# Optimization experiments

Hardware: AMD Instinct MI355X
Metric: run time of the kernel (lower is better)

Reference implementation:

```python
import jax, jax.numpy as jnp
import numpy as np

EPS = 1e-4
MP_SILU_C = 0.596
RES_T = 0.3
ATTN_T = 0.3
CLIP = 256.0
HEADS = 8


def normalize(x, dim, eps=EPS):
    # matches torch normalize: x / (eps + sqrt(norm.numel()/x.numel()) * ||x||_dim)
    norm = jnp.sqrt(jnp.sum(jnp.square(x.astype(jnp.float32)), axis=dim, keepdims=True))
    alpha = np.sqrt(norm.size / x.size)
    return x / (eps + alpha * norm).astype(x.dtype)


def mp_silu(x):
    return jax.nn.silu(x) / MP_SILU_C


def mp_sum(a, b, t):
    return (a * (1.0 - t) + b * t) / np.sqrt((1.0 - t) ** 2 + t ** 2)


def mp_conv(x, w, gain=1.0):
    # weight-normalized conv / linear (eval mode: no in-place weight copy)
    w = w.astype(jnp.float32)
    w = normalize(w, tuple(range(1, w.ndim)))
    fan = int(np.prod(w.shape[1:]))
    w = w * (gain / np.sqrt(fan))
    w = w.astype(x.dtype)
    if w.ndim == 2:
        return x @ w.T
    return jax.lax.conv_general_dilated(
        x, w, window_strides=(1, 1), padding='SAME',
        dimension_numbers=('NCHW', 'OIHW', 'NCHW'))


def setup_inputs() -> dict:
    key = jax.random.key(0)
    ks = jax.random.split(key, 8)
    return {
        'x': jax.random.normal(ks[0], (16, 256, 32, 32), jnp.float32),
        'emb': jax.random.normal(ks[1], (16, 1024), jnp.float32),
        'w_skip': jax.random.normal(ks[2], (512, 256, 1, 1), jnp.float32),
        'w_res0': jax.random.normal(ks[3], (512, 512, 3, 3), jnp.float32),
        'w_emb': jax.random.normal(ks[4], (512, 1024), jnp.float32),
        'w_res1': jax.random.normal(ks[5], (512, 512, 3, 3), jnp.float32),
        'w_qkv': jax.random.normal(ks[6], (1536, 512, 1, 1), jnp.float32),
        'w_proj': jax.random.normal(ks[7], (512, 512, 1, 1), jnp.float32),
        'emb_gain': jnp.zeros([], jnp.float32),
    }


def reference(x, emb, w_skip, w_res0, w_emb, w_res1, w_qkv, w_proj, emb_gain):
    # flavor='enc', resample_mode='keep'
    x = mp_conv(x, w_skip)          # conv_skip (in!=out)
    x = normalize(x, 1)             # pixel norm over channels
    y = mp_conv(mp_silu(x), w_res0)
    c = mp_conv(emb, w_emb, gain=emb_gain) + 1.0   # [N, C]
    y = mp_silu(y * c[:, :, None, None].astype(y.dtype))
    y = mp_conv(y, w_res1)
    x = mp_sum(x, y, RES_T)
    # QK-normalized self-attention over H*W tokens
    N, C, H, W = x.shape
    ch = C // HEADS
    y = mp_conv(x, w_qkv)                              # [N, 3C, H, W]
    y = y.reshape(N, HEADS, ch, 3, H * W)
    qkv = normalize(y, 2)                              # L2-normalize per-head channels
    q, k, v = qkv[:, :, :, 0, :], qkv[:, :, :, 1, :], qkv[:, :, :, 2, :]
    attn = jax.nn.softmax(
        jnp.einsum('nhcq,nhck->nhqk', q, k) / np.sqrt(ch), axis=3)
    y = jnp.einsum('nhqk,nhck->nhcq', attn, v).reshape(N, C, H, W)
    y = mp_conv(y, w_proj)
    x = mp_sum(x, y, ATTN_T)
    return jnp.clip(x, -CLIP, CLIP)
```

## Files before the change

kernel.cpp:

```cpp
#include <hip/hip_runtime.h>

typedef unsigned short u16;
typedef unsigned int   u32;
typedef __attribute__((ext_vector_type(8))) short bf16x8;
typedef __attribute__((ext_vector_type(4))) float f32x4;
typedef __attribute__((ext_vector_type(4))) int   int4v;

#define DEV static __device__ __forceinline__

DEV u16 f2b(float f){ u32 u = __builtin_bit_cast(u32,f); u = (u + 0x7FFFu + ((u>>16)&1u))>>16; return (u16)u; }
DEV float b2f(u16 h){ return __builtin_bit_cast(float,(u32)h<<16); }
DEV float mpsilu(float t){ return t/(1.f+__expf(-t)) * 1.6778523489932886f; }
DEV u32 cvtpk(float lo, float hi){ u32 r; asm("v_cvt_pk_bf16_f32 %0, %1, %2" : "=v"(r) : "v"(lo), "v"(hi)); return r; }

DEV void gload16(void* l, const void* g){
  __builtin_amdgcn_global_load_lds(
    (const __attribute__((address_space(1))) void*)g,
    (__attribute__((address_space(3))) void*)l, 16, 0, 0);
}

#define OFF_W0B    0ull
#define OFF_W1B    4718592ull
#define OFF_WSKIPB 9437184ull
#define OFF_WQKVB  9699328ull
#define OFF_WPROJB 11272192ull
#define OFF_WEMB   11796480ull
#define OFF_CEMB   13893632ull
#define OFF_XSKIP  13926400ull
#define OFF_YATT   13926400ull
#define OFF_XNORM  47480832ull
#define OFF_QKVRAW 47480832ull
#define OFF_PAD0   97812480ull
#define OFF_Q      97812480ull
#define OFF_PAD1   116752384ull
#define OFF_V      116752384ull
#define OFF_XB     135692288ull
#define OFF_XRESB  169246720ull
#define OFF_K      186023936ull

__global__ __launch_bounds__(256) void k_prep_weights(
    const float* __restrict__ w_skip, const float* __restrict__ w_res0,
    const float* __restrict__ w_emb,  const float* __restrict__ w_res1,
    const float* __restrict__ w_qkv,  const float* __restrict__ w_proj,
    const float* __restrict__ egain, char* __restrict__ ws)
{
  int b = blockIdx.x, tid = threadIdx.x, lane = tid&63, wid = tid>>6;
  if(b >= 4096){
    int idx = (b-4096)*256 + tid;
    int4v z = {0,0,0,0};
    for(; idx < 270336; idx += 67584){
      int chunk = idx & 63;
      int rest  = idx >> 6;
      int bp    = rest % 132;
      int rest2 = rest / 132;
      int n     = rest2 & 15;
      int buf   = rest2 >> 4;
      int py, px;
      if(bp < 34){ py=0; px=bp; }
      else if(bp < 68){ py=33; px=bp-34; }
      else if(bp < 100){ py=1+(bp-68); px=0; }
      else { py=1+(bp-100); px=33; }
      char* dst = ws + OFF_PAD0 + (size_t)buf*18939904ull
                + ((size_t)n*1156 + (size_t)py*34 + px)*1024 + (chunk<<4);
      *(int4v*)dst = z;
    }
    return;
  }
  const float* src; int fan, mode, o; u16* dstB=nullptr; float* dstF=nullptr; float gain=1.f;
  if(b<512)       { o=b;      src=w_res0+(size_t)o*4608; fan=4608; mode=1; dstB=(u16*)(ws+OFF_W0B); }
  else if(b<1024) { o=b-512;  src=w_res1+(size_t)o*4608; fan=4608; mode=1; dstB=(u16*)(ws+OFF_W1B); }
  else if(b<1536) { o=b-1024; src=w_skip+(size_t)o*256;  fan=256;  mode=0; dstB=(u16*)(ws+OFF_WSKIPB); }
  else if(b<3072) { o=b-1536; src=w_qkv+(size_t)o*512;   fan=512;  mode=0; dstB=(u16*)(ws+OFF_WQKVB); }
  else if(b<3584) { o=b-3072; src=w_proj+(size_t)o*512;  fan=512;  mode=0; dstB=(u16*)(ws+OFF_WPROJB); }
  else            { o=b-3584; src=w_emb+(size_t)o*1024;  fan=1024; mode=2; dstF=(float*)(ws+OFF_WEMB); gain=*egain; }
  float ss=0;
  for(int i=tid;i<fan;i+=256){ float v=src[i]; ss += v*v; }
  for(int i=1;i<64;i<<=1) ss += __shfl_xor(ss,i);
  __shared__ float red[4];
  if(lane==0) red[wid]=ss;
  __syncthreads();
  ss = red[0]+red[1]+red[2]+red[3];
  float scale = gain / (1e-4f*sqrtf((float)fan) + sqrtf(ss));
  if(mode==1){
    for(int t2=tid;t2<4608;t2+=256){
      int tap=t2>>9, c=t2&511;
      dstB[(size_t)tap*262144 + o*512 + c] = f2b(src[c*9+tap]*scale);
    }
  } else {
    for(int i=tid;i<fan;i+=256){
      float v = src[i]*scale;
      if(mode==0) dstB[(size_t)o*fan + i] = f2b(v);
      else dstF[(size_t)o*1024 + i] = v;
    }
  }
}

__global__ __launch_bounds__(256) void k_emb(const float* __restrict__ emb,
    const float* __restrict__ wembs, float* __restrict__ cemb)
{
  int gw = (blockIdx.x*256 + threadIdx.x)>>6, lane = threadIdx.x&63;
  int n = gw>>9, o = gw&511;
  const float* e = emb + (size_t)n*1024;
  const float* w = wembs + (size_t)o*1024;
  float s=0;
  for(int i=lane*4;i<1024;i+=256){
    float4 a=*(const float4*)(e+i), b=*(const float4*)(w+i);
    s += a.x*b.x + a.y*b.y + a.z*b.z + a.w*b.w;
  }
  for(int i=1;i<64;i<<=1) s += __shfl_xor(s,i);
  if(lane==0) cemb[n*512+o] = s + 1.0f;
}

__global__ __launch_bounds__(256) void k_cast_x(const float* __restrict__ x, u16* __restrict__ xb){
  __shared__ u16 t[64*257];
  int bid=blockIdx.x, tid=threadIdx.x;
  int n=bid>>4, p0=(bid&15)<<6;
  int p=tid&63, c0=tid>>6;
  for(int c=c0;c<256;c+=4)
    t[p*257+c] = f2b(x[((size_t)((n<<8)+c)<<10) + p0 + p]);
  __syncthreads();
  for(int task=tid;task<2048;task+=256){
    int pp=task>>5, oc=(task&31)<<3;
    union{u16 u[8]; int4v v;} pk;
    #pragma unroll
    for(int i=0;i<8;++i) pk.u[i]=t[pp*257+oc+i];
    *(int4v*)(xb + ((size_t)((n<<10)+p0+pp))*256 + oc) = pk.v;
  }
}

__global__ __launch_bounds__(512) void k_gemm(const u16* __restrict__ A, const u16* __restrict__ Bw,
    int K, int ntiles, int mode, u16* __restrict__ out_b,
    const u16* __restrict__ xresb, float* __restrict__ dout)
{
  __shared__ u16 SH[3*24576];
  int bid=blockIdx.x, tid=threadIdx.x;
  int cpx = gridDim.x>>3;
  bid = (bid&7)*cpx + (bid>>3);
  int per_n = ntiles<<2;
  int n = bid/per_n, rem = bid%per_n, mt = rem/ntiles, nt = rem%ntiles;
  int lane=tid&63, wid=tid>>6, lg=lane>>4, li=lane&15;
  int wm=(wid>>1)<<6, wn=(wid&1)<<6;
  f32x4 acc[4][4];
  f32x4 zz = {0.f,0.f,0.f,0.f};
  #pragma unroll
  for(int i=0;i<4;++i) for(int j=0;j<4;++j) acc[i][j]=zz;

  const char* apc = (const char*)(A + (size_t)(n*1024 + mt*256)*K);
  const char* bpc = (const char*)(Bw + (size_t)(nt*128)*K);
  int a_off[4], b_off[2], lofA[4], lofB[2];
  #pragma unroll
  for(int i=0;i<4;++i){
    int c = tid + (i<<9);
    int r = c>>3, sc = (c&7) ^ (r&7);
    lofA[i] = c<<4;
    a_off[i] = (r*K + sc*8)*2;
  }
  #pragma unroll
  for(int i=0;i<2;++i){
    int c = tid + (i<<9);
    int r = c>>3, sc = (c&7) ^ (r&7);
    lofB[i] = 32768 + (c<<4);
    b_off[i] = (r*K + sc*8)*2;
  }
  char* SB = (char*)SH;
  auto STAGE = [&](int step, int buf){
    int so = step<<7;
    char* base = SB + buf*49152;
    #pragma unroll
    for(int i=0;i<4;++i) gload16(base + lofA[i], apc + a_off[i] + so);
    #pragma unroll
    for(int i=0;i<2;++i) gload16(base + lofB[i], bpc + b_off[i] + so);
  };
  int nsteps = K>>6;
  STAGE(0,0); STAGE(1,1);
  int bufsel = 0;
  for(int t=0;t<nsteps;++t){
    if(t < nsteps-1){ asm volatile("s_waitcnt vmcnt(6)" ::: "memory"); }
    else            { asm volatile("s_waitcnt vmcnt(0)" ::: "memory"); }
    __builtin_amdgcn_s_barrier();
    __builtin_amdgcn_sched_barrier(0);
    if(t+2 < nsteps) STAGE(t+2, (t+2)%3);
    const char* Ab = SB + bufsel*49152;
    const char* Bb = Ab + 32768;
    #pragma unroll
    for(int ks=0;ks<2;++ks){
      bf16x8 a[4], b[4];
      int bo = (lg<<4) + (ks<<6);
      #pragma unroll
      for(int i=0;i<4;++i){ int r = wm + (i<<4) + li; a[i] = *(const bf16x8*)(Ab + r*128 + (bo ^ ((r&7)<<4))); }
      #pragma unroll
      for(int j=0;j<4;++j){ int r = wn + (j<<4) + li; b[j] = *(const bf16x8*)(Bb + r*128 + (bo ^ ((r&7)<<4))); }
      __builtin_amdgcn_s_setprio(1);
      #pragma unroll
      for(int i=0;i<4;++i)
        #pragma unroll
        for(int j=0;j<4;++j)
          acc[i][j] = __builtin_amdgcn_mfma_f32_16x16x32_bf16(a[i], b[j], acc[i][j], 0, 0, 0);
      __builtin_amdgcn_s_setprio(0);
    }
    bufsel = (bufsel==2) ? 0 : bufsel+1;
  }

  int N = ntiles<<7;
  #pragma unroll
  for(int mf=0;mf<4;++mf){
    #pragma unroll
    for(int nf=0;nf<4;++nf){
      int oc = nt*128 + wn + (nf<<4) + li;
      #pragma unroll
      for(int jj=0;jj<4;++jj){
        float v = acc[mf][nf][jj];
        int p = mt*256 + wm + (mf<<4) + (lg<<2) + jj;
        size_t idx = (size_t)(n*1024+p)*N + oc;
        if(mode==1) out_b[idx]=f2b(v);
        else{
          float xr = b2f(xresb[(size_t)(n*1024+p)*512 + oc]);
          float r = (xr*0.7f + v*0.3f)*1.3130643285972254f;
          r = fminf(fmaxf(r,-256.f),256.f);
          dout[((size_t)(n*512+oc)<<10) + p] = r;
        }
      }
    }
  }
}

__global__ __launch_bounds__(256) void k_conv3x3(const u16* __restrict__ inpad, const u16* __restrict__ wt,
    int mode, const float* __restrict__ cemb, const u16* __restrict__ xnormb,
    u16* __restrict__ ypad, u16* __restrict__ xresb)
{
  __shared__ char SB[61440];
  int bid=blockIdx.x, tid=threadIdx.x;
  bid = (bid&7)*64 + (bid>>3);
  int n=bid>>5, rem=bid&31, mt=rem>>2, nt=rem&3;
  int lane=tid&63, wid=tid>>6, lg=lane>>4, li=lane&15;
  int wm=(wid>>1)<<6, wn=(wid&1)<<6;
  int mt4 = mt<<2;
  f32x4 acc[4][4];
  f32x4 zz={0.f,0.f,0.f,0.f};
  #pragma unroll
  for(int i=0;i<4;++i)
    #pragma unroll
    for(int j=0;j<4;++j) acc[i][j]=zz;

  const char* ipc = (const char*)(inpad + (size_t)n*591872);
  const char* wtc = (const char*)wt;
  int abase[4];
  #pragma unroll
  for(int i=0;i<4;++i){ int r = wm + (i<<4) + li; abase[i] = (r>>5)*34 + (r&31); }

  auto STAGE_B = [&](int tap, int kc, int buf){
    int off = tap*524288 + (kc<<7);
    char* base = SB + 28672 + buf*16384;
    #pragma unroll
    for(int i=0;i<4;++i){
      int c = tid + (i<<8);
      int r = c>>3, sc = ((c&7) ^ (r&7))<<4;
      gload16(base + (c<<4), wtc + (nt*128+r)*1024 + sc + off);
    }
  };
  auto STAGE_A = [&](int kcn){
    #pragma unroll
    for(int i=0;i<7;++i){
      int c = tid + (i<<8);
      int slot = c>>3; if(slot>203) slot=203;
      int scol = ((c&7) ^ (slot&7))<<4;
      int py = (slot*241)>>13;
      int px = slot - py*34;
      gload16(SB + (c<<4), ipc + (size_t)((mt4+py)*34+px)*1024 + (kcn<<7) + scol);
    }
  };
  bf16x8 ar[2][4];
  auto LOAD_A = [&](int tap){
    int dy = (tap*11)>>5;
    int dd = dy*34 + (tap - dy*3);
    #pragma unroll
    for(int ks=0;ks<2;++ks){
      int bo = (lg<<4) + (ks<<6);
      #pragma unroll
      for(int i=0;i<4;++i){
        int slot = abase[i] + dd;
        ar[ks][i] = *(const bf16x8*)(SB + slot*128 + (bo ^ ((slot&7)<<4)));
      }
    }
  };

  STAGE_A(0);
  STAGE_B(0,0,0);
  int bbuf = 0;
  for(int kc=0;kc<8;++kc){
    #pragma unroll
    for(int tap=0;tap<9;++tap){
      if(tap==8){ asm volatile("s_waitcnt vmcnt(0) lgkmcnt(0)" ::: "memory"); }
      else      { asm volatile("s_waitcnt vmcnt(0)" ::: "memory"); }
      __builtin_amdgcn_s_barrier();
      __builtin_amdgcn_sched_barrier(0);
      if(tap==8){
        if(kc<7){ STAGE_A(kc+1); STAGE_B(0, kc+1, bbuf^1); }
      } else {
        STAGE_B(tap+1, kc, bbuf^1);
      }
      if(tap==0) LOAD_A(0);
      const char* Bb = SB + 28672 + bbuf*16384;
      #pragma unroll
      for(int ks=0;ks<2;++ks){
        bf16x8 b[4];
        int bo = (lg<<4) + (ks<<6);
        #pragma unroll
        for(int j=0;j<4;++j){ int r = wn + (j<<4) + li; b[j] = *(const bf16x8*)(Bb + r*128 + (bo ^ ((r&7)<<4))); }
        __builtin_amdgcn_s_setprio(1);
        #pragma unroll
        for(int i=0;i<4;++i)
          #pragma unroll
          for(int j=0;j<4;++j)
            acc[i][j] = __builtin_amdgcn_mfma_f32_16x16x32_bf16(ar[ks][i], b[j], acc[i][j], 0, 0, 0);
        __builtin_amdgcn_s_setprio(0);
      }
      if(tap<8) LOAD_A(tap+1);
      bbuf ^= 1;
    }
  }

  #pragma unroll
  for(int mf=0;mf<4;++mf){
    #pragma unroll
    for(int nf=0;nf<4;++nf){
      int oc = nt*128 + wn + (nf<<4) + li;
      float ce = (mode==0) ? cemb[n*512+oc] : 0.f;
      #pragma unroll
      for(int jj=0;jj<4;++jj){
        float v = acc[mf][nf][jj];
        int p = mt*128 + wm + (mf<<4) + (lg<<2) + jj;
        int py=p>>5, px=p&31;
        if(mode==0){
          float s = mpsilu(v*ce);
          ypad[((size_t)n*1156 + (size_t)(py+1)*34 + (px+1))*512 + oc] = f2b(s);
        }else{
          size_t ix = (size_t)(n*1024+p)*512 + oc;
          float r = (b2f(xnormb[ix])*0.7f + v*0.3f)*1.3130643285972254f;
          xresb[ix]=f2b(r);
        }
      }
    }
  }
}

__global__ __launch_bounds__(256) void k_pixnorm(const u16* __restrict__ xs,
    u16* __restrict__ xn, u16* __restrict__ pad0)
{
  int tid=threadIdx.x, lane=tid&63, wid=tid>>6;
  for(int p = blockIdx.x*4 + wid; p < 16384; p += gridDim.x*4){
    union{u16 u[8]; int4v v;} in;
    in.v = *(const int4v*)(xs + (size_t)p*512 + lane*8);
    float f[8]; float ss=0.f;
    #pragma unroll
    for(int i=0;i<8;++i){ f[i]=b2f(in.u[i]); ss += f[i]*f[i]; }
    for(int i=1;i<64;i<<=1) ss += __shfl_xor(ss,i);
    float sc = 1.f/(1e-4f + sqrtf(ss)*0.04419417382415922f);
    union{u16 u[8]; int4v v;} on, op;
    #pragma unroll
    for(int i=0;i<8;++i){ float v=f[i]*sc; on.u[i]=f2b(v); op.u[i]=f2b(mpsilu(v)); }
    *(int4v*)(xn + (size_t)p*512 + lane*8) = on.v;
    int n=p>>10, py=(p>>5)&31, px=p&31;
    u16* pd = pad0 + ((size_t)n*1156 + (size_t)(py+1)*34 + (px+1))*512;
    *(int4v*)(pd + lane*8) = op.v;
  }
}

__global__ __launch_bounds__(256) void k_qkv_norm(const u16* __restrict__ raw,
    u16* __restrict__ q, u16* __restrict__ k, u16* __restrict__ v)
{
  __shared__ u16 lraw[8*1536];
  __shared__ float lscale[192];
  int bid=blockIdx.x, tid=threadIdx.x;
  int n=bid>>7, p0=(bid&127)<<3;
  for(int cc=tid; cc<1536; cc+=256){
    int pix=cc/192, off=(cc%192)<<3;
    *(int4v*)(lraw + pix*1536 + off) = *(const int4v*)(raw + ((size_t)((n<<10)+p0+pix))*1536 + off);
  }
  __syncthreads();
  if(tid<192){
    int pix=tid/24, rem=tid%24, h=rem/3, w=rem%3;
    const u16* r = lraw + pix*1536 + h*192 + w;
    float ss=0;
    #pragma unroll
    for(int c=0;c<64;++c){ float f=b2f(r[c*3]); ss += f*f; }
    lscale[tid] = 1.f/(1e-4f + sqrtf(ss)*0.125f);
  }
  __syncthreads();
  for(int t=tid;t<512;t+=256){
    int pix=t>>6, h=(t>>3)&7, oct=(t&7)<<3;
    float sq=lscale[pix*24+h*3+0]*0.18033688011112043f;
    float sk=lscale[pix*24+h*3+1];
    const u16* r = lraw + pix*1536 + h*192;
    union{u16 u[8]; int4v vv;} pq, pk;
    #pragma unroll
    for(int i=0;i<8;++i){ int c=oct+i; pq.u[i]=f2b(b2f(r[3*c+0])*sq); pk.u[i]=f2b(b2f(r[3*c+1])*sk); }
    size_t base = ((size_t)((n<<3)+h)<<10) + p0 + pix;
    *(int4v*)(q + base*64 + oct) = pq.vv;
    *(int4v*)(k + base*64 + oct) = pk.vv;
  }
  for(int t=tid;t<512;t+=256){
    int h=t>>6, c=t&63;
    union{u16 u[8]; int4v vv;} pv;
    #pragma unroll
    for(int pix=0;pix<8;++pix)
      pv.u[pix] = f2b(b2f(lraw[pix*1536 + h*192 + 3*c + 2]) * lscale[pix*24+h*3+2]);
    *(int4v*)(v + (((size_t)((n<<3)+h)<<6) + c)*1024 + p0) = pv.vv;
  }
}

__global__ __launch_bounds__(512) void k_attn(const u16* __restrict__ Q, const u16* __restrict__ Kb,
    const u16* __restrict__ Vb, u16* __restrict__ yatt)
{
  __shared__ char lds[65536];
  __shared__ float alds[8][32];
  int bid=blockIdx.x, tid=threadIdx.x;
  int pair = (bid&7)*16 + (bid>>5);
  int qt2 = (bid>>3)&3;
  int n=pair>>3, h=pair&7;
  const char* qb = (const char*)(Q  + ((size_t)pair*1024 + qt2*256)*64);
  const char* kb = (const char*)(Kb + (size_t)pair*1024*64);
  const char* vb = (const char*)(Vb + (size_t)pair*64*1024);
  int lane=tid&63, wid=tid>>6, lg=lane>>4, li=lane&15;
  int wq=wid<<5;
  char* Pt = lds + 32768;

  #pragma unroll
  for(int i=0;i<4;++i){
    int c = lane + (i<<6);
    int r = wq + (c>>3);
    int sc = ((c&7) ^ (r&7))<<4;
    gload16(Pt + (wq<<7) + (c<<4), qb + (size_t)r*128 + sc);
  }
  asm volatile("s_waitcnt vmcnt(0)" ::: "memory");
  bf16x8 bq[2][2];
  #pragma unroll
  for(int qq=0;qq<2;++qq)
    #pragma unroll
    for(int ks=0;ks<2;++ks){
      int r=wq+(qq<<4)+li; int bo=(lg<<4)+(ks<<6);
      bq[qq][ks]=*(const bf16x8*)(Pt + r*128 + (bo ^ ((r&7)<<4)));
    }
  asm volatile("s_waitcnt lgkmcnt(0)" ::: "memory");
  __builtin_amdgcn_sched_barrier(0);

  auto STAGE = [&](int kt, int buf){
    char* kd = lds + buf*16384;
    { int c = tid; int r = c>>3; int sc = ((c&7) ^ (r&7))<<4;
      gload16(kd + (c<<4), kb + (size_t)kt*8192 + (r<<7) + sc); }
    { int c = tid; int r = c>>3; int sc = ((c&7) ^ (r&7))<<4;
      gload16(kd + 8192 + (c<<4), vb + (size_t)r*2048 + kt*128 + sc); }
  };
  STAGE(0,0);

  f32x4 o0[2][4];
  float m0=-1e30f, m1=-1e30f, l0=0.f, l1=0.f;
  f32x4 zz={0.f,0.f,0.f,0.f};
  #pragma unroll
  for(int i=0;i<2;++i) for(int j=0;j<4;++j) o0[i][j]=zz;

  for(int kt=0;kt<16;++kt){
    asm volatile("s_waitcnt vmcnt(0)" ::: "memory");
    __builtin_amdgcn_s_barrier();
    __builtin_amdgcn_sched_barrier(0);
    if(kt<15) STAGE(kt+1, (kt+1)&1);
    const char* Kt = lds + (kt&1)*16384;
    const char* Vt = Kt + 8192;
    f32x4 s[4][2];
    #pragma unroll
    for(int i=0;i<4;++i){ s[i][0]=zz; s[i][1]=zz; }
    #pragma unroll
    for(int ks=0;ks<2;++ks){
      int bo=(lg<<4)+(ks<<6);
      bf16x8 a[4];
      #pragma unroll
      for(int kk=0;kk<4;++kk){ int r=(kk<<4)+li; a[kk]=*(const bf16x8*)(Kt + r*128 + (bo ^ ((r&7)<<4))); }
      __builtin_amdgcn_s_setprio(1);
      #pragma unroll
      for(int kk=0;kk<4;++kk)
        #pragma unroll
        for(int qq=0;qq<2;++qq)
          s[kk][qq] = __builtin_amdgcn_mfma_f32_16x16x32_bf16(a[kk], bq[qq][ks], s[kk][qq], 0,0,0);
      __builtin_amdgcn_s_setprio(0);
    }
    float pm0=-1e30f, pm1=-1e30f;
    #pragma unroll
    for(int kk=0;kk<4;++kk)
      #pragma unroll
      for(int jj=0;jj<4;++jj){ pm0=fmaxf(pm0,s[kk][0][jj]); pm1=fmaxf(pm1,s[kk][1][jj]); }
    pm0=fmaxf(pm0,__shfl_xor(pm0,16)); pm0=fmaxf(pm0,__shfl_xor(pm0,32));
    pm1=fmaxf(pm1,__shfl_xor(pm1,16)); pm1=fmaxf(pm1,__shfl_xor(pm1,32));
    if(!__all((pm0 <= m0+11.5f) && (pm1 <= m1+11.5f))){
      float mn0=fmaxf(m0,pm0), mn1=fmaxf(m1,pm1);
      float al0=__builtin_amdgcn_exp2f(m0-mn0), al1=__builtin_amdgcn_exp2f(m1-mn1);
      if(lg==0){ alds[wid][li]=al0; alds[wid][16+li]=al1; }
      m0=mn0; m1=mn1; l0*=al0; l1*=al1;
      #pragma unroll
      for(int mf=0;mf<2;++mf)
        #pragma unroll
        for(int jj=0;jj<4;++jj){
          float am = alds[wid][(mf<<4)+(lg<<2)+jj];
          #pragma unroll
          for(int cf=0;cf<4;++cf) o0[mf][cf][jj]*=am;
        }
    }
    float rs0=0.f, rs1=0.f;
    #pragma unroll
    for(int kk=0;kk<4;++kk)
      #pragma unroll
      for(int jj=0;jj<4;++jj){
        float p0=__builtin_amdgcn_exp2f(s[kk][0][jj]-m0); s[kk][0][jj]=p0; rs0+=p0;
        float p1=__builtin_amdgcn_exp2f(s[kk][1][jj]-m1); s[kk][1][jj]=p1; rs1+=p1;
      }
    rs0+=__shfl_xor(rs0,16); rs0+=__shfl_xor(rs0,32);
    rs1+=__shfl_xor(rs1,16); rs1+=__shfl_xor(rs1,32);
    l0+=rs0; l1+=rs1;
    #pragma unroll
    for(int qq=0;qq<2;++qq){
      int q = wq+(qq<<4)+li;
      int rsw = (q&7)<<4;
      #pragma unroll
      for(int kk=0;kk<4;++kk){
        uint2 w;
        w.x = cvtpk(s[kk][qq][0], s[kk][qq][1]);
        w.y = cvtpk(s[kk][qq][2], s[kk][qq][3]);
        int bo = ((kk<<5)+(lg<<3)) ^ rsw;
        *(uint2*)(Pt + q*128 + bo) = w;
      }
    }
    #pragma unroll
    for(int ks=0;ks<2;++ks){
      int bo=(lg<<4)+(ks<<6);
      bf16x8 a[2], b[4];
      #pragma unroll
      for(int i=0;i<2;++i){ int r=wq+(i<<4)+li; a[i]=*(const bf16x8*)(Pt + r*128 + (bo ^ ((r&7)<<4))); }
      #pragma unroll
      for(int j=0;j<4;++j){ int r=(j<<4)+li;    b[j]=*(const bf16x8*)(Vt + r*128 + (bo ^ ((r&7)<<4))); }
      __builtin_amdgcn_s_setprio(1);
      #pragma unroll
      for(int i=0;i<2;++i)
        #pragma unroll
        for(int j=0;j<4;++j)
          o0[i][j] = __builtin_amdgcn_mfma_f32_16x16x32_bf16(a[i], b[j], o0[i][j], 0,0,0);
      __builtin_amdgcn_s_setprio(0);
    }
  }
  if(lg==0){ alds[wid][li]=1.f/l0; alds[wid][16+li]=1.f/l1; }
  #pragma unroll
  for(int mf=0;mf<2;++mf)
    #pragma unroll
    for(int jj=0;jj<4;++jj){
      float rl = alds[wid][(mf<<4)+(lg<<2)+jj];
      int p=(qt2<<8)+wq+(mf<<4)+(lg<<2)+jj;
      #pragma unroll
      for(int nf=0;nf<4;++nf){
        int c=(nf<<4)+li;
        yatt[((size_t)(n*1024)+p)*512 + (h<<6) + c] = f2b(o0[mf][nf][jj]*rl);
      }
    }
}

extern "C" void kernel_launch(void* const* d_in, const int* in_sizes, int n_in,
                              void* d_out, int out_size, void* d_ws, size_t ws_size,
                              hipStream_t stream)
{
  (void)in_sizes; (void)n_in; (void)out_size; (void)ws_size;
  const float* x      = (const float*)d_in[0];
  const float* emb    = (const float*)d_in[1];
  const float* w_skip = (const float*)d_in[2];
  const float* w_res0 = (const float*)d_in[3];
  const float* w_emb  = (const float*)d_in[4];
  const float* w_res1 = (const float*)d_in[5];
  const float* w_qkv  = (const float*)d_in[6];
  const float* w_proj = (const float*)d_in[7];
  const float* egain  = (const float*)d_in[8];
  char* ws = (char*)d_ws;
  float* dout = (float*)d_out;

  u16* w0b    = (u16*)(ws+OFF_W0B);
  u16* w1b    = (u16*)(ws+OFF_W1B);
  u16* wskipb = (u16*)(ws+OFF_WSKIPB);
  u16* wqkvb  = (u16*)(ws+OFF_WQKVB);
  u16* wprojb = (u16*)(ws+OFF_WPROJB);
  float* wembs= (float*)(ws+OFF_WEMB);
  float* cemb = (float*)(ws+OFF_CEMB);
  u16* xskipb = (u16*)(ws+OFF_XSKIP);
  u16* yatt   = (u16*)(ws+OFF_YATT);
  u16* xnormb = (u16*)(ws+OFF_XNORM);
  u16* qkvraw = (u16*)(ws+OFF_QKVRAW);
  u16* pad0   = (u16*)(ws+OFF_PAD0);
  u16* qbuf   = (u16*)(ws+OFF_Q);
  u16* pad1   = (u16*)(ws+OFF_PAD1);
  u16* vbuf   = (u16*)(ws+OFF_V);
  u16* xb     = (u16*)(ws+OFF_XB);
  u16* xresb  = (u16*)(ws+OFF_XRESB);
  u16* kbuf   = (u16*)(ws+OFF_K);

  hipLaunchKernelGGL(k_prep_weights, dim3(4360), dim3(256), 0, stream,
                     w_skip, w_res0, w_emb, w_res1, w_qkv, w_proj, egain, ws);
  hipLaunchKernelGGL(k_emb, dim3(2048), dim3(256), 0, stream, emb, wembs, cemb);
  hipLaunchKernelGGL(k_cast_x, dim3(256), dim3(256), 0, stream, x, xb);
  hipLaunchKernelGGL(k_gemm, dim3(256), dim3(512), 0, stream,
                     xb, wskipb, 256, 4, 1, xskipb, (const u16*)nullptr, (float*)nullptr);
  hipLaunchKernelGGL(k_pixnorm, dim3(1024), dim3(256), 0, stream, xskipb, xnormb, pad0);
  hipLaunchKernelGGL(k_conv3x3, dim3(512), dim3(256), 0, stream,
                     pad0, w0b, 0, cemb, (const u16*)nullptr, pad1, (u16*)nullptr);
  hipLaunchKernelGGL(k_conv3x3, dim3(512), dim3(256), 0, stream,
                     pad1, w1b, 1, (const float*)nullptr, xnormb, (u16*)nullptr, xresb);
  hipLaunchKernelGGL(k_gemm, dim3(768), dim3(512), 0, stream,
                     xresb, wqkvb, 512, 12, 1, qkvraw, (const u16*)nullptr, (float*)nullptr);
  hipLaunchKernelGGL(k_qkv_norm, dim3(2048), dim3(256), 0, stream, qkvraw, qbuf, kbuf, vbuf);
  hipLaunchKernelGGL(k_attn, dim3(512), dim3(512), 0, stream, qbuf, kbuf, vbuf, yatt);
  hipLaunchKernelGGL(k_gemm, dim3(256), dim3(512), 0, stream,
                     yatt, wprojb, 512, 4, 2, (u16*)nullptr, xresb, dout);
}
```

Baseline: 412.9 us.

## Fuse QKV normalization into QKV GEMM epilogue and emb weight-norm into k_emb

Result: faster. 347.8 us (-15.8%).

```diff
diff --git a/kernel.cpp b/kernel.cpp
--- a/kernel.cpp
+++ b/kernel.cpp
@@ -24,12 +24,10 @@
 #define OFF_WSKIPB 9437184ull
 #define OFF_WQKVB  9699328ull
 #define OFF_WPROJB 11272192ull
-#define OFF_WEMB   11796480ull
 #define OFF_CEMB   13893632ull
 #define OFF_XSKIP  13926400ull
 #define OFF_YATT   13926400ull
 #define OFF_XNORM  47480832ull
-#define OFF_QKVRAW 47480832ull
 #define OFF_PAD0   97812480ull
 #define OFF_Q      97812480ull
 #define OFF_PAD1   116752384ull
@@ -40,13 +38,12 @@
 
 __global__ __launch_bounds__(256) void k_prep_weights(
     const float* __restrict__ w_skip, const float* __restrict__ w_res0,
-    const float* __restrict__ w_emb,  const float* __restrict__ w_res1,
-    const float* __restrict__ w_qkv,  const float* __restrict__ w_proj,
-    const float* __restrict__ egain, char* __restrict__ ws)
+    const float* __restrict__ w_res1, const float* __restrict__ w_qkv,
+    const float* __restrict__ w_proj, char* __restrict__ ws)
 {
   int b = blockIdx.x, tid = threadIdx.x, lane = tid&63, wid = tid>>6;
-  if(b >= 4096){
-    int idx = (b-4096)*256 + tid;
+  if(b >= 3584){
+    int idx = (b-3584)*256 + tid;
     int4v z = {0,0,0,0};
     for(; idx < 270336; idx += 67584){
       int chunk = idx & 63;
@@ -66,13 +63,12 @@
     }
     return;
   }
-  const float* src; int fan, mode, o; u16* dstB=nullptr; float* dstF=nullptr; float gain=1.f;
+  const float* src; int fan, mode, o; u16* dstB=nullptr;
   if(b<512)       { o=b;      src=w_res0+(size_t)o*4608; fan=4608; mode=1; dstB=(u16*)(ws+OFF_W0B); }
   else if(b<1024) { o=b-512;  src=w_res1+(size_t)o*4608; fan=4608; mode=1; dstB=(u16*)(ws+OFF_W1B); }
   else if(b<1536) { o=b-1024; src=w_skip+(size_t)o*256;  fan=256;  mode=0; dstB=(u16*)(ws+OFF_WSKIPB); }
-  else if(b<3072) { o=b-1536; src=w_qkv+(size_t)o*512;   fan=512;  mode=0; dstB=(u16*)(ws+OFF_WQKVB); }
-  else if(b<3584) { o=b-3072; src=w_proj+(size_t)o*512;  fan=512;  mode=0; dstB=(u16*)(ws+OFF_WPROJB); }
-  else            { o=b-3584; src=w_emb+(size_t)o*1024;  fan=1024; mode=2; dstF=(float*)(ws+OFF_WEMB); gain=*egain; }
+  else if(b<3072) { o=b-1536; src=w_qkv+(size_t)o*512;   fan=512;  mode=2; dstB=(u16*)(ws+OFF_WQKVB); }
+  else            { o=b-3072; src=w_proj+(size_t)o*512;  fan=512;  mode=0; dstB=(u16*)(ws+OFF_WPROJB); }
   float ss=0;
   for(int i=tid;i<fan;i+=256){ float v=src[i]; ss += v*v; }
   for(int i=1;i<64;i<<=1) ss += __shfl_xor(ss,i);
@@ -80,35 +76,42 @@
   if(lane==0) red[wid]=ss;
   __syncthreads();
   ss = red[0]+red[1]+red[2]+red[3];
-  float scale = gain / (1e-4f*sqrtf((float)fan) + sqrtf(ss));
+  float scale = 1.f / (1e-4f*sqrtf((float)fan) + sqrtf(ss));
   if(mode==1){
     for(int t2=tid;t2<4608;t2+=256){
       int tap=t2>>9, c=t2&511;
       dstB[(size_t)tap*262144 + o*512 + c] = f2b(src[c*9+tap]*scale);
     }
+  } else if(mode==2){
+    int h = o/192, rem = o - h*192, c = rem/3, w = rem - c*3;
+    int onew = h*192 + w*64 + c;
+    for(int i=tid;i<512;i+=256)
+      dstB[(size_t)onew*512 + i] = f2b(src[i]*scale);
   } else {
-    for(int i=tid;i<fan;i+=256){
-      float v = src[i]*scale;
-      if(mode==0) dstB[(size_t)o*fan + i] = f2b(v);
-      else dstF[(size_t)o*1024 + i] = v;
-    }
+    for(int i=tid;i<fan;i+=256)
+      dstB[(size_t)o*fan + i] = f2b(src[i]*scale);
   }
 }
 
 __global__ __launch_bounds__(256) void k_emb(const float* __restrict__ emb,
-    const float* __restrict__ wembs, float* __restrict__ cemb)
+    const float* __restrict__ wemb, const float* __restrict__ egain,
+    float* __restrict__ cemb)
 {
   int gw = (blockIdx.x*256 + threadIdx.x)>>6, lane = threadIdx.x&63;
   int n = gw>>9, o = gw&511;
   const float* e = emb + (size_t)n*1024;
-  const float* w = wembs + (size_t)o*1024;
-  float s=0;
+  const float* w = wemb + (size_t)o*1024;
+  float s=0, ssw=0;
   for(int i=lane*4;i<1024;i+=256){
     float4 a=*(const float4*)(e+i), b=*(const float4*)(w+i);
-    s += a.x*b.x + a.y*b.y + a.z*b.z + a.w*b.w;
-  }
-  for(int i=1;i<64;i<<=1) s += __shfl_xor(s,i);
-  if(lane==0) cemb[n*512+o] = s + 1.0f;
+    s   += a.x*b.x + a.y*b.y + a.z*b.z + a.w*b.w;
+    ssw += b.x*b.x + b.y*b.y + b.z*b.z + b.w*b.w;
+  }
+  for(int i=1;i<64;i<<=1){ s += __shfl_xor(s,i); ssw += __shfl_xor(ssw,i); }
+  if(lane==0){
+    float scale = (*egain) / (1e-4f*32.0f + sqrtf(ssw));
+    cemb[n*512+o] = s*scale + 1.0f;
+  }
 }
 
 __global__ __launch_bounds__(256) void k_cast_x(const float* __restrict__ x, u16* __restrict__ xb){
@@ -130,7 +133,8 @@
 
 __global__ __launch_bounds__(512) void k_gemm(const u16* __restrict__ A, const u16* __restrict__ Bw,
     int K, int ntiles, int mode, u16* __restrict__ out_b,
-    const u16* __restrict__ xresb, float* __restrict__ dout)
+    const u16* __restrict__ xresb, float* __restrict__ dout,
+    u16* __restrict__ qd, u16* __restrict__ kd, u16* __restrict__ vd)
 {
   __shared__ u16 SH[3*24576];
   int bid=blockIdx.x, tid=threadIdx.x;
@@ -201,6 +205,41 @@
     bufsel = (bufsel==2) ? 0 : bufsel+1;
   }
 
+  if(mode==3){
+    int g = (nt*128 + wn)>>6;
+    int h = g/3, w = g - h*3;
+    size_t pair = (size_t)(n*8 + h);
+    #pragma unroll
+    for(int mf=0;mf<4;++mf){
+      #pragma unroll
+      for(int jj=0;jj<4;++jj){
+        float ssq = 0.f;
+        #pragma unroll
+        for(int nf=0;nf<4;++nf){ float t2=acc[mf][nf][jj]; ssq += t2*t2; }
+        ssq += __shfl_xor(ssq,1); ssq += __shfl_xor(ssq,2);
+        ssq += __shfl_xor(ssq,4); ssq += __shfl_xor(ssq,8);
+        float sc = 1.f/(1e-4f + sqrtf(ssq)*0.125f);
+        if(w==0) sc *= 0.18033688011112043f;
+        int p = mt*256 + wm + (mf<<4) + (lg<<2) + jj;
+        if(w==2){
+          #pragma unroll
+          for(int nf=0;nf<4;++nf){
+            int c=(nf<<4)+li;
+            vd[pair*65536 + (size_t)c*1024 + p] = f2b(acc[mf][nf][jj]*sc);
+          }
+        }else{
+          u16* dst = (w==0) ? qd : kd;
+          #pragma unroll
+          for(int nf=0;nf<4;++nf){
+            int c=(nf<<4)+li;
+            dst[(pair*1024 + p)*64 + c] = f2b(acc[mf][nf][jj]*sc);
+          }
+        }
+      }
+    }
+    return;
+  }
+
   int N = ntiles<<7;
   #pragma unroll
   for(int mf=0;mf<4;++mf){
@@ -288,7 +327,6 @@
   STAGE_B(0,0,0);
   int bbuf = 0;
   for(int kc=0;kc<8;++kc){
-    #pragma unroll
     for(int tap=0;tap<9;++tap){
       if(tap==8){ asm volatile("s_waitcnt vmcnt(0) lgkmcnt(0)" ::: "memory"); }
       else      { asm volatile("s_waitcnt vmcnt(0)" ::: "memory"); }
@@ -363,49 +401,6 @@
     int n=p>>10, py=(p>>5)&31, px=p&31;
     u16* pd = pad0 + ((size_t)n*1156 + (size_t)(py+1)*34 + (px+1))*512;
     *(int4v*)(pd + lane*8) = op.v;
-  }
-}
-
-__global__ __launch_bounds__(256) void k_qkv_norm(const u16* __restrict__ raw,
-    u16* __restrict__ q, u16* __restrict__ k, u16* __restrict__ v)
-{
-  __shared__ u16 lraw[8*1536];
-  __shared__ float lscale[192];
-  int bid=blockIdx.x, tid=threadIdx.x;
-  int n=bid>>7, p0=(bid&127)<<3;
-  for(int cc=tid; cc<1536; cc+=256){
-    int pix=cc/192, off=(cc%192)<<3;
-    *(int4v*)(lraw + pix*1536 + off) = *(const int4v*)(raw + ((size_t)((n<<10)+p0+pix))*1536 + off);
-  }
-  __syncthreads();
-  if(tid<192){
-    int pix=tid/24, rem=tid%24, h=rem/3, w=rem%3;
-    const u16* r = lraw + pix*1536 + h*192 + w;
-    float ss=0;
-    #pragma unroll
-    for(int c=0;c<64;++c){ float f=b2f(r[c*3]); ss += f*f; }
-    lscale[tid] = 1.f/(1e-4f + sqrtf(ss)*0.125f);
-  }
-  __syncthreads();
-  for(int t=tid;t<512;t+=256){
-    int pix=t>>6, h=(t>>3)&7, oct=(t&7)<<3;
-    float sq=lscale[pix*24+h*3+0]*0.18033688011112043f;
-    float sk=lscale[pix*24+h*3+1];
-    const u16* r = lraw + pix*1536 + h*192;
-    union{u16 u[8]; int4v vv;} pq, pk;
-    #pragma unroll
-    for(int i=0;i<8;++i){ int c=oct+i; pq.u[i]=f2b(b2f(r[3*c+0])*sq); pk.u[i]=f2b(b2f(r[3*c+1])*sk); }
-    size_t base = ((size_t)((n<<3)+h)<<10) + p0 + pix;
-    *(int4v*)(q + base*64 + oct) = pq.vv;
-    *(int4v*)(k + base*64 + oct) = pk.vv;
-  }
-  for(int t=tid;t<512;t+=256){
-    int h=t>>6, c=t&63;
-    union{u16 u[8]; int4v vv;} pv;
-    #pragma unroll
-    for(int pix=0;pix<8;++pix)
-      pv.u[pix] = f2b(b2f(lraw[pix*1536 + h*192 + 3*c + 2]) * lscale[pix*24+h*3+2]);
-    *(int4v*)(v + (((size_t)((n<<3)+h)<<6) + c)*1024 + p0) = pv.vv;
   }
 }
 
@@ -582,12 +577,10 @@
   u16* wskipb = (u16*)(ws+OFF_WSKIPB);
   u16* wqkvb  = (u16*)(ws+OFF_WQKVB);
   u16* wprojb = (u16*)(ws+OFF_WPROJB);
-  float* wembs= (float*)(ws+OFF_WEMB);
   float* cemb = (float*)(ws+OFF_CEMB);
   u16* xskipb = (u16*)(ws+OFF_XSKIP);
   u16* yatt   = (u16*)(ws+OFF_YATT);
   u16* xnormb = (u16*)(ws+OFF_XNORM);
-  u16* qkvraw = (u16*)(ws+OFF_QKVRAW);
   u16* pad0   = (u16*)(ws+OFF_PAD0);
   u16* qbuf   = (u16*)(ws+OFF_Q);
   u16* pad1   = (u16*)(ws+OFF_PAD1);
@@ -596,21 +589,23 @@
   u16* xresb  = (u16*)(ws+OFF_XRESB);
   u16* kbuf   = (u16*)(ws+OFF_K);
 
-  hipLaunchKernelGGL(k_prep_weights, dim3(4360), dim3(256), 0, stream,
-                     w_skip, w_res0, w_emb, w_res1, w_qkv, w_proj, egain, ws);
-  hipLaunchKernelGGL(k_emb, dim3(2048), dim3(256), 0, stream, emb, wembs, cemb);
+  hipLaunchKernelGGL(k_prep_weights, dim3(3848), dim3(256), 0, stream,
+                     w_skip, w_res0, w_res1, w_qkv, w_proj, ws);
+  hipLaunchKernelGGL(k_emb, dim3(2048), dim3(256), 0, stream, emb, w_emb, egain, cemb);
   hipLaunchKernelGGL(k_cast_x, dim3(256), dim3(256), 0, stream, x, xb);
   hipLaunchKernelGGL(k_gemm, dim3(256), dim3(512), 0, stream,
-                     xb, wskipb, 256, 4, 1, xskipb, (const u16*)nullptr, (float*)nullptr);
+                     xb, wskipb, 256, 4, 1, xskipb, (const u16*)nullptr, (float*)nullptr,
+                     (u16*)nullptr, (u16*)nullptr, (u16*)nullptr);
   hipLaunchKernelGGL(k_pixnorm, dim3(1024), dim3(256), 0, stream, xskipb, xnormb, pad0);
   hipLaunchKernelGGL(k_conv3x3, dim3(512), dim3(256), 0, stream,
                      pad0, w0b, 0, cemb, (const u16*)nullptr, pad1, (u16*)nullptr);
   hipLaunchKernelGGL(k_conv3x3, dim3(512), dim3(256), 0, stream,
                      pad1, w1b, 1, (const float*)nullptr, xnormb, (u16*)nullptr, xresb);
   hipLaunchKernelGGL(k_gemm, dim3(768), dim3(512), 0, stream,
-                     xresb, wqkvb, 512, 12, 1, qkvraw, (const u16*)nullptr, (float*)nullptr);
-  hipLaunchKernelGGL(k_qkv_norm, dim3(2048), dim3(256), 0, stream, qkvraw, qbuf, kbuf, vbuf);
+                     xresb, wqkvb, 512, 12, 3, (u16*)nullptr, (const u16*)nullptr, (float*)nullptr,
+                     qbuf, kbuf, vbuf);
   hipLaunchKernelGGL(k_attn, dim3(512), dim3(512), 0, stream, qbuf, kbuf, vbuf, yatt);
   hipLaunchKernelGGL(k_gemm, dim3(256), dim3(512), 0, stream,
-                     yatt, wprojb, 512, 4, 2, (u16*)nullptr, xresb, dout);
-}
+                     yatt, wprojb, 512, 4, 2, (u16*)nullptr, xresb, dout,
+                     (u16*)nullptr, (u16*)nullptr, (u16*)nullptr);
+}
```
